# Optimization experiments

Measured on AMD Instinct MI355X. Metric: run time of the kernel, lower is better.

Reference implementation:

```python
import jax, jax.numpy as jnp
import numpy as np

L, ND, ED, AD = 2, 128, 64, 64
N, E, A, G = 50000, 300000, 600000, 16
EPS = 1e-5


def _graph_norm(h, batch, num_graphs, w, b):
    # PyG LayerNorm(mode='graph'): scalar mean/var over all nodes*features per graph.
    F = h.shape[-1]
    cnt = jax.ops.segment_sum(jnp.ones(h.shape[0], h.dtype), batch, num_segments=num_graphs)
    norm = jnp.maximum(cnt, 1.0) * F  # [G]
    mean = (jax.ops.segment_sum(h, batch, num_segments=num_graphs).sum(-1) / norm)[batch][:, None]
    hc = h - mean
    var = (jax.ops.segment_sum(hc * hc, batch, num_segments=num_graphs).sum(-1) / norm)
    out = hc * jax.lax.rsqrt(var + EPS)[batch][:, None]
    return out * w + b


def setup_inputs() -> dict:
    key = jax.random.key(0)
    ks = jax.random.split(key, 24)

    def lin(k, fi, fo):
        return jax.random.normal(k, (L, fi, fo), jnp.float32) / jnp.sqrt(float(fi))

    inp = {
        "x": jax.random.normal(ks[0], (N, ND), jnp.float32),
        "edge_attr": jax.random.normal(ks[1], (E, ED), jnp.float32),
        "angle_attr": jax.random.normal(ks[2], (A, AD), jnp.float32),
        # node_edge_mlp: [2*ND+ED -> ED], plain linear (plain_last=True)
        "W_ne": lin(ks[3], 2 * ND + ED, ED), "b_ne": jnp.zeros((L, ED), jnp.float32),
        "g_e": jnp.ones((L, ED), jnp.float32), "be_e": jnp.zeros((L, ED), jnp.float32),
        # edge_angle_mlp: [2*ED+AD -> AD]
        "W_ea": lin(ks[4], 2 * ED + AD, AD), "b_ea": jnp.zeros((L, AD), jnp.float32),
        "g_a": jnp.ones((L, AD), jnp.float32), "be_a": jnp.zeros((L, AD), jnp.float32),
        # edge_graph_mp message net: [2*ED+AD -> ED]
        "W_emp": lin(ks[5], 2 * ED + AD, ED), "b_emp": jnp.zeros((L, ED), jnp.float32),
        "g_emp": jnp.ones((L, ED), jnp.float32), "be_emp": jnp.zeros((L, ED), jnp.float32),
        # node_graph_mp message net: [2*ND+ED -> ND]
        "W_nmp": lin(ks[6], 2 * ND + ED, ND), "b_nmp": jnp.zeros((L, ND), jnp.float32),
        "g_nmp": jnp.ones((L, ND), jnp.float32), "be_nmp": jnp.zeros((L, ND), jnp.float32),
        "node_batch": jnp.sort(jax.random.randint(ks[7], (N,), 0, G)),
        "edge_index": jax.random.randint(ks[8], (2, E), 0, N),
        "edge_batch": jnp.sort(jax.random.randint(ks[9], (E,), 0, G)),
        "threebody_index": jax.random.randint(ks[10], (2, A), 0, E),
        "angle_batch": jnp.sort(jax.random.randint(ks[11], (A,), 0, G)),
        "num_graphs": G,
    }
    return inp


def reference(x, edge_attr, angle_attr,
              W_ne, b_ne, g_e, be_e,
              W_ea, b_ea, g_a, be_a,
              W_emp, b_emp, g_emp, be_emp,
              W_nmp, b_nmp, g_nmp, be_nmp,
              node_batch, edge_index, edge_batch,
              threebody_index, angle_batch, num_graphs):
    src_e, dst_e = edge_index[0], edge_index[1]
    src_t, dst_t = threebody_index[0], threebody_index[1]
    n_nodes, n_edges = x.shape[0], edge_attr.shape[0]
    for i in range(W_ne.shape[0]):
        # node-pair -> edge update + residual + graph norm
        ecat = jnp.concatenate([x[src_e], x[dst_e], edge_attr], axis=-1)
        edge_attr = edge_attr + ecat @ W_ne[i] + b_ne[i]
        edge_attr = _graph_norm(edge_attr, edge_batch, num_graphs, g_e[i], be_e[i])
        # edge-pair -> angle update + residual + graph norm
        acat = jnp.concatenate([edge_attr[src_t], edge_attr[dst_t], angle_attr], axis=-1)
        angle_attr = angle_attr + acat @ W_ea[i] + b_ea[i]
        angle_attr = _graph_norm(angle_attr, angle_batch, num_graphs, g_a[i], be_a[i])
        # edge_graph_mp: angle-mediated message passing over edges
        mcat = jnp.concatenate([edge_attr[src_t], edge_attr[dst_t], angle_attr], axis=-1)
        msg = jax.nn.relu(mcat @ W_emp[i] + b_emp[i])
        agg = jax.ops.segment_sum(msg, dst_t, num_segments=n_edges)
        edge_attr = _graph_norm(edge_attr + agg, edge_batch, num_graphs, g_emp[i], be_emp[i])
        # node_graph_mp: edge-mediated message passing over nodes
        ncat = jnp.concatenate([x[src_e], x[dst_e], edge_attr], axis=-1)
        nmsg = jax.nn.relu(ncat @ W_nmp[i] + b_nmp[i])
        nagg = jax.ops.segment_sum(nmsg, dst_e, num_segments=n_nodes)
        x = _graph_norm(x + nagg, node_batch, num_graphs, g_nmp[i], be_nmp[i])
    return x
```

## Files before the change

kernel.cpp:

```cpp
#include <hip/hip_runtime.h>

typedef __attribute__((ext_vector_type(8))) short bf16x8_t;
typedef __attribute__((ext_vector_type(4))) short bf16x4_t;
typedef __attribute__((ext_vector_type(4))) float f32x4_t;

constexpr int NG = 16;
constexpr float EPS = 1e-5f;

__device__ inline unsigned short f2bf(float f) {
  unsigned u = __builtin_bit_cast(unsigned, f);
  u += 0x7FFFu + ((u >> 16) & 1u);
  return (unsigned short)(u >> 16);
}
__device__ inline float bf2f(unsigned short u) {
  unsigned x = ((unsigned)u) << 16;
  return __builtin_bit_cast(float, x);
}

__global__ __launch_bounds__(256) void k_dense_x(
    const float* __restrict__ x,
    const unsigned short* __restrict__ WtNE,
    const unsigned short* __restrict__ WtNM,
    unsigned short* __restrict__ P, int nN)
{
  int gw = (int)((blockIdx.x * 256u + threadIdx.x) >> 6);
  int ntile = nN >> 4;
  if (gw >= ntile) return;
  int lane = threadIdx.x & 63;
  int colb = lane & 15;
  int ko = (lane >> 4) << 3;
  int rowb = (lane >> 4) << 2;
  int row = (gw << 4) + colb;
  const float* xr = x + (size_t)row * 128;
  f32x4_t a1[4] = {}, a2[4] = {}, a3[8] = {}, a4[8] = {};
#pragma unroll
  for (int c = 0; c < 4; ++c) {
    float4 f0 = *(const float4*)(xr + c * 32 + ko);
    float4 f1 = *(const float4*)(xr + c * 32 + ko + 4);
    float vv[8] = {f0.x,f0.y,f0.z,f0.w,f1.x,f1.y,f1.z,f1.w};
    bf16x8_t a;
#pragma unroll
    for (int k = 0; k < 8; ++k) a[k] = (short)f2bf(vv[k]);
#pragma unroll
    for (int nb = 0; nb < 4; ++nb) {
      bf16x8_t b1 = *(const bf16x8_t*)(WtNE + (size_t)(nb * 16 + colb) * 320 + c * 32 + ko);
      a1[nb] = __builtin_amdgcn_mfma_f32_16x16x32_bf16(a, b1, a1[nb], 0, 0, 0);
      bf16x8_t b2 = *(const bf16x8_t*)(WtNE + (size_t)(nb * 16 + colb) * 320 + (c + 4) * 32 + ko);
      a2[nb] = __builtin_amdgcn_mfma_f32_16x16x32_bf16(a, b2, a2[nb], 0, 0, 0);
    }
#pragma unroll
    for (int nb = 0; nb < 8; ++nb) {
      bf16x8_t b3 = *(const bf16x8_t*)(WtNM + (size_t)(nb * 16 + colb) * 320 + c * 32 + ko);
      a3[nb] = __builtin_amdgcn_mfma_f32_16x16x32_bf16(a, b3, a3[nb], 0, 0, 0);
      bf16x8_t b4 = *(const bf16x8_t*)(WtNM + (size_t)(nb * 16 + colb) * 320 + (c + 4) * 32 + ko);
      a4[nb] = __builtin_amdgcn_mfma_f32_16x16x32_bf16(a, b4, a4[nb], 0, 0, 0);
    }
  }
#pragma unroll
  for (int r = 0; r < 4; ++r) {
    size_t ro = (size_t)((gw << 4) + rowb + r) * 384;
    bf16x4_t t1, t2;
#pragma unroll
    for (int nb = 0; nb < 4; ++nb) { t1[nb] = (short)f2bf(a1[nb][r]); t2[nb] = (short)f2bf(a2[nb][r]); }
    *(bf16x4_t*)(P + ro + colb * 4) = t1;
    *(bf16x4_t*)(P + ro + 64 + colb * 4) = t2;
    bf16x8_t t3, t4;
#pragma unroll
    for (int nb = 0; nb < 8; ++nb) { t3[nb] = (short)f2bf(a3[nb][r]); t4[nb] = (short)f2bf(a4[nb][r]); }
    *(bf16x8_t*)(P + ro + 128 + colb * 8) = t3;
    *(bf16x8_t*)(P + ro + 256 + colb * 8) = t4;
  }
}

__global__ __launch_bounds__(256) void k_edge(
    const unsigned short* __restrict__ P, const float* e_in, float* e_out,
    const int* __restrict__ ei, const int* __restrict__ ebatch,
    const unsigned short* __restrict__ Wt,
    const float* __restrict__ bias,
    const float* __restrict__ afA, const float* __restrict__ afB,
    float* __restrict__ gs1, float* __restrict__ gs2,
    unsigned short* __restrict__ pn, int nE)
{
  __shared__ float lA[1024], lB[1024];
  __shared__ float ls1[NG], ls2[NG];
  for (int i = threadIdx.x; i < 1024; i += 256) { lA[i] = afA[i]; lB[i] = afB[i]; }
  if (threadIdx.x < NG) { ls1[threadIdx.x] = 0.f; ls2[threadIdx.x] = 0.f; }
  __syncthreads();
  int gw = (int)((blockIdx.x * 256u + threadIdx.x) >> 6);
  int ntile = nE >> 4;
  bool act = gw < ntile;
  int lane = threadIdx.x & 63;
  int colb = lane & 15;
  int ko = (lane >> 4) << 3;
  int rowb = (lane >> 4) << 2;
  float sr[4] = {0.f,0.f,0.f,0.f}, ssr[4] = {0.f,0.f,0.f,0.f};
  if (act) {
    int sI[4], dI[4];
#pragma unroll
    for (int r = 0; r < 4; ++r) {
      int e_r = (gw << 4) + rowb + r;
      sI[r] = ei[e_r]; dI[r] = ei[nE + e_r];
    }
    bf16x4_t g1[4], g2[4]; bf16x8_t g3[4], g4[4];
#pragma unroll
    for (int r = 0; r < 4; ++r) {
      g1[r] = *(const bf16x4_t*)(P + (size_t)sI[r] * 384 + colb * 4);
      g2[r] = *(const bf16x4_t*)(P + (size_t)dI[r] * 384 + 64 + colb * 4);
      g3[r] = *(const bf16x8_t*)(P + (size_t)sI[r] * 384 + 128 + colb * 8);
      g4[r] = *(const bf16x8_t*)(P + (size_t)dI[r] * 384 + 256 + colb * 8);
    }
    int row = (gw << 4) + colb;
    int ge = ebatch[row];
    const float* er = e_in + (size_t)row * 64;
    f32x4_t acc[4] = {};
#pragma unroll
    for (int c2 = 0; c2 < 2; ++c2) {
      int fb = c2 * 32 + ko;
      float4 f0 = *(const float4*)(er + fb);
      float4 f1 = *(const float4*)(er + fb + 4);
      float vv[8] = {f0.x,f0.y,f0.z,f0.w,f1.x,f1.y,f1.z,f1.w};
      bf16x8_t a;
#pragma unroll
      for (int k = 0; k < 8; ++k) a[k] = (short)f2bf(vv[k] * lA[ge*64 + fb + k] + lB[ge*64 + fb + k]);
#pragma unroll
      for (int nb = 0; nb < 4; ++nb) {
        bf16x8_t b = *(const bf16x8_t*)(Wt + (size_t)(nb * 16 + colb) * 320 + (8 + c2) * 32 + ko);
        acc[nb] = __builtin_amdgcn_mfma_f32_16x16x32_bf16(a, b, acc[nb], 0, 0, 0);
      }
    }
#pragma unroll
    for (int r = 0; r < 4; ++r) {
      int e_ = (gw << 4) + rowb + r;
      int gr = ebatch[e_];
#pragma unroll
      for (int nb = 0; nb < 4; ++nb) {
        int col = nb * 16 + colb;
        size_t off = (size_t)e_ * 64 + col;
        float vv = e_in[off] * lA[gr*64 + col] + lB[gr*64 + col] + bias[col]
                 + acc[nb][r] + bf2f((unsigned short)g1[r][nb]) + bf2f((unsigned short)g2[r][nb]);
        e_out[off] = vv;
        sr[r] += vv; ssr[r] += vv * vv;
      }
      bf16x8_t pv;
#pragma unroll
      for (int k = 0; k < 8; ++k)
        pv[k] = (short)f2bf(bf2f((unsigned short)g3[r][k]) + bf2f((unsigned short)g4[r][k]));
      *(bf16x8_t*)(pn + (size_t)e_ * 128 + colb * 8) = pv;
    }
  }
#pragma unroll
  for (int m = 1; m <= 8; m <<= 1)
#pragma unroll
    for (int r = 0; r < 4; ++r) { sr[r] += __shfl_xor(sr[r], m); ssr[r] += __shfl_xor(ssr[r], m); }
  if (act && colb == 0) {
#pragma unroll
    for (int r = 0; r < 4; ++r) {
      int g = ebatch[(gw << 4) + rowb + r];
      atomicAdd(&ls1[g], sr[r]); atomicAdd(&ls2[g], ssr[r]);
    }
  }
  __syncthreads();
  if (threadIdx.x < NG) {
    atomicAdd(&gs1[threadIdx.x], ls1[threadIdx.x]);
    atomicAdd(&gs2[threadIdx.x], ls2[threadIdx.x]);
  }
}

__global__ __launch_bounds__(256) void k_fin_nmp(
    const float* __restrict__ e, const int* __restrict__ ebatch,
    const unsigned short* __restrict__ Wt,
    const float* __restrict__ bias,
    const float* __restrict__ afEA, const float* __restrict__ afEB,
    const unsigned short* __restrict__ pn,
    unsigned short* __restrict__ msg, int nE)
{
  __shared__ float lEA[1024], lEB[1024];
  for (int i = threadIdx.x; i < 1024; i += 256) { lEA[i] = afEA[i]; lEB[i] = afEB[i]; }
  __syncthreads();
  int gw = (int)((blockIdx.x * 256u + threadIdx.x) >> 6);
  int ntile = nE >> 4;
  if (gw >= ntile) return;
  int lane = threadIdx.x & 63;
  int colb = lane & 15;
  int ko = (lane >> 4) << 3;
  int rowb = (lane >> 4) << 2;
  int row = (gw << 4) + colb;
  int ge = ebatch[row];
  const float* er = e + (size_t)row * 64;
  f32x4_t acc[8] = {};
#pragma unroll
  for (int c2 = 0; c2 < 2; ++c2) {
    int fb = c2 * 32 + ko;
    float4 f0 = *(const float4*)(er + fb);
    float4 f1 = *(const float4*)(er + fb + 4);
    float vv[8] = {f0.x,f0.y,f0.z,f0.w,f1.x,f1.y,f1.z,f1.w};
    bf16x8_t a;
#pragma unroll
    for (int k = 0; k < 8; ++k) a[k] = (short)f2bf(vv[k] * lEA[ge*64 + fb + k] + lEB[ge*64 + fb + k]);
#pragma unroll
    for (int nb = 0; nb < 8; ++nb) {
      bf16x8_t b = *(const bf16x8_t*)(Wt + (size_t)(nb * 16 + colb) * 320 + (8 + c2) * 32 + ko);
      acc[nb] = __builtin_amdgcn_mfma_f32_16x16x32_bf16(a, b, acc[nb], 0, 0, 0);
    }
  }
#pragma unroll
  for (int r = 0; r < 4; ++r) {
    int e_ = (gw << 4) + rowb + r;
    bf16x8_t p8 = *(const bf16x8_t*)(pn + (size_t)e_ * 128 + colb * 8);
#pragma unroll
    for (int nb = 0; nb < 8; ++nb) {
      int col = nb * 16 + colb;
      float v = fmaxf(acc[nb][r] + bf2f((unsigned short)p8[nb]) + bias[col], 0.f);
      msg[(size_t)e_ * 128 + col] = f2bf(v);
    }
  }
}

__global__ __launch_bounds__(256) void k_mm_angle(
    const unsigned short* __restrict__ eB1, const float* a_in, float* a_out,
    const int* __restrict__ ti, const int* __restrict__ abatch,
    const unsigned short* __restrict__ Wt, const float* __restrict__ bias,
    const float* __restrict__ afAA, const float* __restrict__ afAB,
    float* __restrict__ gs1, float* __restrict__ gs2, int nA)
{
  __shared__ float lAA[1024], lAB[1024];
  __shared__ float ls1[NG], ls2[NG];
  for (int i = threadIdx.x; i < 1024; i += 256) { lAA[i] = afAA[i]; lAB[i] = afAB[i]; }
  if (threadIdx.x < NG) { ls1[threadIdx.x] = 0.f; ls2[threadIdx.x] = 0.f; }
  __syncthreads();
  int gw = (int)((blockIdx.x * 256u + threadIdx.x) >> 6);
  int ntile = nA >> 4;
  bool act = gw < ntile;
  int lane = threadIdx.x & 63;
  int colb = lane & 15;
  int ko = (lane >> 4) << 3;
  int rowb = (lane >> 4) << 2;
  float sr[4] = {0.f,0.f,0.f,0.f}, ssr[4] = {0.f,0.f,0.f,0.f};
  if (act) {
    int row = (gw << 4) + colb;
    int s = ti[row], d = ti[nA + row];
    int ga = abatch[row];
    const unsigned short* es = eB1 + (size_t)s * 64;
    const unsigned short* ed = eB1 + (size_t)d * 64;
    const float* ar = a_in + (size_t)row * 64;
    f32x4_t acc[4] = {};
#pragma unroll
    for (int c = 0; c < 6; ++c) {
      bf16x8_t a;
      if (c < 4) {
        const unsigned short* bp = (c < 2) ? es + c * 32 : ed + (c - 2) * 32;
        a = *(const bf16x8_t*)(bp + ko);
      } else {
        int fb = (c - 4) * 32 + ko;
        float4 f0 = *(const float4*)(ar + fb);
        float4 f1 = *(const float4*)(ar + fb + 4);
        float vv[8] = {f0.x,f0.y,f0.z,f0.w,f1.x,f1.y,f1.z,f1.w};
#pragma unroll
        for (int k = 0; k < 8; ++k) a[k] = (short)f2bf(vv[k] * lAA[ga*64 + fb + k] + lAB[ga*64 + fb + k]);
      }
#pragma unroll
      for (int nb = 0; nb < 4; ++nb) {
        bf16x8_t b = *(const bf16x8_t*)(Wt + (size_t)(nb * 16 + colb) * 192 + c * 32 + ko);
        acc[nb] = __builtin_amdgcn_mfma_f32_16x16x32_bf16(a, b, acc[nb], 0, 0, 0);
      }
    }
#pragma unroll
    for (int r = 0; r < 4; ++r) {
      int a_ = (gw << 4) + rowb + r;
      int gr = abatch[a_];
#pragma unroll
      for (int nb = 0; nb < 4; ++nb) {
        int col = nb * 16 + colb;
        size_t off = (size_t)a_ * 64 + col;
        float vv = a_in[off] * lAA[gr*64 + col] + lAB[gr*64 + col] + bias[col] + acc[nb][r];
        a_out[off] = vv;
        sr[r] += vv; ssr[r] += vv * vv;
      }
    }
  }
#pragma unroll
  for (int m = 1; m <= 8; m <<= 1)
#pragma unroll
    for (int r = 0; r < 4; ++r) { sr[r] += __shfl_xor(sr[r], m); ssr[r] += __shfl_xor(ssr[r], m); }
  if (act && colb == 0) {
#pragma unroll
    for (int r = 0; r < 4; ++r) {
      int g = abatch[(gw << 4) + rowb + r];
      atomicAdd(&ls1[g], sr[r]); atomicAdd(&ls2[g], ssr[r]);
    }
  }
  __syncthreads();
  if (threadIdx.x < NG) {
    atomicAdd(&gs1[threadIdx.x], ls1[threadIdx.x]);
    atomicAdd(&gs2[threadIdx.x], ls2[threadIdx.x]);
  }
}

__global__ __launch_bounds__(256) void k_mm_emp(
    const unsigned short* __restrict__ eB1, const float* __restrict__ a_,
    const int* __restrict__ ti, const int* __restrict__ abatch,
    const unsigned short* __restrict__ Wt, const float* __restrict__ bias,
    const float* __restrict__ afAA, const float* __restrict__ afAB,
    unsigned short* __restrict__ msg, int nA)
{
  __shared__ float lAA[1024], lAB[1024];
  for (int i = threadIdx.x; i < 1024; i += 256) { lAA[i] = afAA[i]; lAB[i] = afAB[i]; }
  __syncthreads();
  int gw = (int)((blockIdx.x * 256u + threadIdx.x) >> 6);
  int ntile = nA >> 4;
  if (gw >= ntile) return;
  int lane = threadIdx.x & 63;
  int colb = lane & 15;
  int ko = (lane >> 4) << 3;
  int rowb = (lane >> 4) << 2;
  int row = (gw << 4) + colb;
  int s = ti[row], d = ti[nA + row];
  int ga = abatch[row];
  const unsigned short* es = eB1 + (size_t)s * 64;
  const unsigned short* ed = eB1 + (size_t)d * 64;
  const float* ar = a_ + (size_t)row * 64;
  f32x4_t acc[4] = {};
#pragma unroll
  for (int c = 0; c < 6; ++c) {
    bf16x8_t a;
    if (c < 4) {
      const unsigned short* bp = (c < 2) ? es + c * 32 : ed + (c - 2) * 32;
      a = *(const bf16x8_t*)(bp + ko);
    } else {
      int fb = (c - 4) * 32 + ko;
      float4 f0 = *(const float4*)(ar + fb);
      float4 f1 = *(const float4*)(ar + fb + 4);
      float vv[8] = {f0.x,f0.y,f0.z,f0.w,f1.x,f1.y,f1.z,f1.w};
#pragma unroll
      for (int k = 0; k < 8; ++k) a[k] = (short)f2bf(vv[k] * lAA[ga*64 + fb + k] + lAB[ga*64 + fb + k]);
    }
#pragma unroll
    for (int nb = 0; nb < 4; ++nb) {
      bf16x8_t b = *(const bf16x8_t*)(Wt + (size_t)(nb * 16 + colb) * 192 + c * 32 + ko);
      acc[nb] = __builtin_amdgcn_mfma_f32_16x16x32_bf16(a, b, acc[nb], 0, 0, 0);
    }
  }
#pragma unroll
  for (int r = 0; r < 4; ++r) {
    int a_idx = (gw << 4) + rowb + r;
#pragma unroll
    for (int nb = 0; nb < 4; ++nb) {
      int col = nb * 16 + colb;
      float v = fmaxf(acc[nb][r] + bias[col], 0.f);
      msg[(size_t)a_idx * 64 + col] = f2bf(v);
    }
  }
}

__global__ __launch_bounds__(256) void k_red_e(
    const unsigned short* __restrict__ msg, const float* e_in, float* e_out,
    const int* __restrict__ ptr, const int* __restrict__ perm,
    const int* __restrict__ ebatch,
    const float* __restrict__ afA, const float* __restrict__ afB,
    float* __restrict__ gs1, float* __restrict__ gs2, int nE)
{
  __shared__ float lA[1024], lB[1024], ls1[NG], ls2[NG];
  for (int i = threadIdx.x; i < 1024; i += 256) { lA[i] = afA[i]; lB[i] = afB[i]; }
  if (threadIdx.x < NG) { ls1[threadIdx.x] = 0.f; ls2[threadIdx.x] = 0.f; }
  __syncthreads();
  int lane = threadIdx.x & 63;
  int wv = (int)((blockIdx.x * 256u + threadIdx.x) >> 6);
  int nw = (int)((gridDim.x * 256u) >> 6);
  for (int eidx = wv; eidx < nE; eidx += nw) {
    int p0 = ptr[eidx], p1 = ptr[eidx + 1];
    float sum = 0.f;
    for (int j = p0; j < p1; ++j) {
      int aidx = perm[j];
      sum += bf2f(msg[(size_t)aidx * 64 + lane]);
    }
    int g = ebatch[eidx];
    size_t off = (size_t)eidx * 64 + lane;
    float v = e_in[off] * lA[g*64 + lane] + lB[g*64 + lane] + sum;
    e_out[off] = v;
    float s = v, ss = v * v;
#pragma unroll
    for (int m = 1; m < 64; m <<= 1) { s += __shfl_xor(s, m); ss += __shfl_xor(ss, m); }
    if (lane == 0) { atomicAdd(&ls1[g], s); atomicAdd(&ls2[g], ss); }
  }
  __syncthreads();
  if (threadIdx.x < NG) {
    atomicAdd(&gs1[threadIdx.x], ls1[threadIdx.x]);
    atomicAdd(&gs2[threadIdx.x], ls2[threadIdx.x]);
  }
}

__global__ __launch_bounds__(256) void k_red_n(
    const unsigned short* __restrict__ msg, const float* x_in, float* out,
    const int* __restrict__ ptr, const int* __restrict__ perm,
    const int* __restrict__ nbatch,
    float* __restrict__ gs1, float* __restrict__ gs2, int nN)
{
  __shared__ float ls1[NG], ls2[NG];
  if (threadIdx.x < NG) { ls1[threadIdx.x] = 0.f; ls2[threadIdx.x] = 0.f; }
  __syncthreads();
  int lane = threadIdx.x & 63;
  int wv = (int)((blockIdx.x * 256u + threadIdx.x) >> 6);
  int nw = (int)((gridDim.x * 256u) >> 6);
  for (int n = wv; n < nN; n += nw) {
    int p0 = ptr[n], p1 = ptr[n + 1];
    float s0 = 0.f, s1v = 0.f;
    for (int j = p0; j < p1; ++j) {
      int e = perm[j];
      unsigned u = *(const unsigned*)(msg + (size_t)e * 128 + lane * 2);
      s0 += bf2f((unsigned short)(u & 0xffffu));
      s1v += bf2f((unsigned short)(u >> 16));
    }
    size_t off = (size_t)n * 128 + lane * 2;
    float h0 = x_in[off] + s0, h1 = x_in[off + 1] + s1v;
    out[off] = h0; out[off + 1] = h1;
    float s = h0 + h1, ss = h0 * h0 + h1 * h1;
#pragma unroll
    for (int m = 1; m < 64; m <<= 1) { s += __shfl_xor(s, m); ss += __shfl_xor(ss, m); }
    if (lane == 0) { int g = nbatch[n]; atomicAdd(&ls1[g], s); atomicAdd(&ls2[g], ss); }
  }
  __syncthreads();
  if (threadIdx.x < NG) {
    atomicAdd(&gs1[threadIdx.x], ls1[threadIdx.x]);
    atomicAdd(&gs2[threadIdx.x], ls2[threadIdx.x]);
  }
}

__global__ __launch_bounds__(256) void k_mkaff(
    const float* __restrict__ s1, const float* __restrict__ s2,
    const float* __restrict__ cnt, int F,
    const float* __restrict__ w, const float* __restrict__ b,
    float* __restrict__ A, float* __restrict__ B)
{
  int idx = blockIdx.x * 256 + threadIdx.x;
  if (idx >= NG * F) return;
  int g = idx / F, f = idx - g * F;
  float norm = fmaxf(cnt[g], 1.f) * (float)F;
  float m = s1[g] / norm;
  float var = s2[g] / norm - m * m;
  float inv = rsqrtf(var + EPS);
  float a = inv * w[f];
  A[idx] = a;
  B[idx] = b[f] - m * a;
}

__global__ __launch_bounds__(256) void k_idaff(float* __restrict__ A, float* __restrict__ B, int n)
{
  int idx = blockIdx.x * 256 + threadIdx.x;
  if (idx < n) { A[idx] = 1.f; B[idx] = 0.f; }
}

__global__ __launch_bounds__(256) void k_norm_ebf(
    const float* __restrict__ e, const int* __restrict__ ebatch,
    const float* __restrict__ afA, const float* __restrict__ afB,
    unsigned short* __restrict__ eB, int nE)
{
  int total = nE * 8;
  int stride = gridDim.x * 256;
  for (int idx = blockIdx.x * 256 + threadIdx.x; idx < total; idx += stride) {
    int row = idx >> 3, q = (idx & 7) * 8;
    int g = ebatch[row];
    const float* er = e + (size_t)row * 64 + q;
    float4 f0 = *(const float4*)er;
    float4 f1 = *(const float4*)(er + 4);
    float vv[8] = {f0.x,f0.y,f0.z,f0.w,f1.x,f1.y,f1.z,f1.w};
    bf16x8_t o;
#pragma unroll
    for (int k = 0; k < 8; ++k) o[k] = (short)f2bf(vv[k] * afA[g*64 + q + k] + afB[g*64 + q + k]);
    *(bf16x8_t*)(eB + (size_t)row * 64 + q) = o;
  }
}

__global__ __launch_bounds__(256) void k_apply(
    float* h, const int* __restrict__ batch,
    const float* __restrict__ A, const float* __restrict__ B, int nN)
{
  int total = nN * 16;
  int stride = gridDim.x * 256;
  for (int idx = blockIdx.x * 256 + threadIdx.x; idx < total; idx += stride) {
    int row = idx >> 4, q = (idx & 15) * 8;
    int g = batch[row];
    float* hp = h + (size_t)row * 128 + q;
    float4 f0 = *(const float4*)hp;
    float4 f1 = *(const float4*)(hp + 4);
    float vv[8] = {f0.x,f0.y,f0.z,f0.w,f1.x,f1.y,f1.z,f1.w};
#pragma unroll
    for (int k = 0; k < 8; ++k) vv[k] = vv[k] * A[(g << 7) + q + k] + B[(g << 7) + q + k];
    float4 g0 = {vv[0],vv[1],vv[2],vv[3]}, g1 = {vv[4],vv[5],vv[6],vv[7]};
    *(float4*)hp = g0;
    *(float4*)(hp + 4) = g1;
  }
}

__global__ __launch_bounds__(256) void k_count(
    const int* __restrict__ batch, int n, float* __restrict__ cnt)
{
  __shared__ float lc[NG];
  if (threadIdx.x < NG) lc[threadIdx.x] = 0.f;
  __syncthreads();
  for (int i = blockIdx.x * 256 + threadIdx.x; i < n; i += gridDim.x * 256)
    atomicAdd(&lc[batch[i]], 1.f);
  __syncthreads();
  if (threadIdx.x < NG) atomicAdd(&cnt[threadIdx.x], lc[threadIdx.x]);
}

__global__ __launch_bounds__(256) void k_hist(
    const int* __restrict__ dst, int n, int* __restrict__ cnt)
{
  for (int i = blockIdx.x * 256 + threadIdx.x; i < n; i += gridDim.x * 256)
    atomicAdd(&cnt[dst[i]], 1);
}

__global__ __launch_bounds__(256) void k_scan1(
    const int* __restrict__ in, int* __restrict__ out, int* __restrict__ bsum, int n)
{
  __shared__ int wtot[4];
  int tid = threadIdx.x, lane = tid & 63, wid = tid >> 6;
  int base = blockIdx.x * 1024 + tid * 4;
  int v[4];
#pragma unroll
  for (int k = 0; k < 4; ++k) v[k] = (base + k < n) ? in[base + k] : 0;
  int tsum = v[0] + v[1] + v[2] + v[3];
  int incl = tsum;
// ... 64 lines not shown
    const int* __restrict__ dst, int* __restrict__ cur, int* __restrict__ perm, int n)
{
  for (int i = blockIdx.x * 256 + threadIdx.x; i < n; i += gridDim.x * 256) {
    int d = dst[i];
    int p = atomicAdd(&cur[d], 1);
    perm[p] = i;
  }
}

__global__ __launch_bounds__(256) void k_wt(
    const float* __restrict__ W, unsigned short* __restrict__ Wt, int K, int NO)
{
  int idx = blockIdx.x * 256 + threadIdx.x;
  if (idx >= K * NO) return;
  int k = idx / NO, j = idx - k * NO;
  Wt[(size_t)j * K + k] = f2bf(W[idx]);
}

extern "C" void kernel_launch(void* const* d_in, const int* in_sizes, int n_in,
                              void* d_out, int out_size, void* d_ws, size_t ws_size,
                              hipStream_t stream)
{
  const float* x0    = (const float*)d_in[0];
  const float* e0    = (const float*)d_in[1];
  const float* a0    = (const float*)d_in[2];
  const float* W_ne  = (const float*)d_in[3];
  const float* b_ne  = (const float*)d_in[4];
  const float* g_e   = (const float*)d_in[5];
  const float* be_e  = (const float*)d_in[6];
  const float* W_ea  = (const float*)d_in[7];
  const float* b_ea  = (const float*)d_in[8];
  const float* g_a   = (const float*)d_in[9];
  const float* be_a  = (const float*)d_in[10];
  const float* W_emp = (const float*)d_in[11];
  const float* b_emp = (const float*)d_in[12];
  const float* g_emp = (const float*)d_in[13];
  const float* be_emp= (const float*)d_in[14];
  const float* W_nmp = (const float*)d_in[15];
  const float* b_nmp = (const float*)d_in[16];
  const float* g_nmp = (const float*)d_in[17];
  const float* be_nmp= (const float*)d_in[18];
  const int* node_batch  = (const int*)d_in[19];
  const int* edge_index  = (const int*)d_in[20];
  const int* edge_batch  = (const int*)d_in[21];
  const int* tb_index    = (const int*)d_in[22];
  const int* angle_batch = (const int*)d_in[23];

  const int N = in_sizes[0] / 128;
  const int E = in_sizes[1] / 64;
  const int A = in_sizes[2] / 64;

  char* wsp = (char*)d_ws;
  auto alloc = [&](size_t bytes) { char* p = wsp; wsp += (bytes + 255) & ~(size_t)255; return p; };
  float*          eA     = (float*)alloc((size_t)E * 64 * 4);
  float*          aA     = (float*)alloc((size_t)A * 64 * 4);
  unsigned short* msg    = (unsigned short*)alloc((size_t)A * 64 * 2);
  unsigned short* pn     = (unsigned short*)alloc((size_t)E * 128 * 2);
  unsigned short* eB1    = (unsigned short*)alloc((size_t)E * 64 * 2);
  int* ptr_n  = (int*)alloc((size_t)(N + 1) * 4);
  int* cur_n  = (int*)alloc((size_t)N * 4);
  int* perm_n = (int*)alloc((size_t)E * 4);
  int* ptr_e  = (int*)alloc((size_t)(E + 1) * 4);
  int* cur_e  = (int*)alloc((size_t)E * 4);
  int* perm_e = (int*)alloc((size_t)A * 4);
  int* bsum   = (int*)alloc(4096 * 4);
  float* stats = (float*)alloc(5 * NG * 4);
  float* s1    = stats;
  float* s2    = stats + NG;
  float* cnt_n = stats + 2 * NG;
  float* cnt_e = stats + 3 * NG;
  float* cnt_a = stats + 4 * NG;
  float* afE_idA = (float*)alloc(1024 * 4); float* afE_idB = (float*)alloc(1024 * 4);
  float* afA_idA = (float*)alloc(1024 * 4); float* afA_idB = (float*)alloc(1024 * 4);
  float* afE1A   = (float*)alloc(1024 * 4); float* afE1B   = (float*)alloc(1024 * 4);
  float* afE2A   = (float*)alloc(1024 * 4); float* afE2B   = (float*)alloc(1024 * 4);
  float* afA1A   = (float*)alloc(1024 * 4); float* afA1B   = (float*)alloc(1024 * 4);
  float* afXA    = (float*)alloc(2048 * 4); float* afXB    = (float*)alloc(2048 * 4);
  unsigned short* wt_ne  = (unsigned short*)alloc((size_t)2 * 320 * 64 * 2);
  unsigned short* wt_ea  = (unsigned short*)alloc((size_t)2 * 192 * 64 * 2);
  unsigned short* wt_emp = (unsigned short*)alloc((size_t)2 * 192 * 64 * 2);
  unsigned short* wt_nmp = (unsigned short*)alloc((size_t)2 * 320 * 128 * 2);

  unsigned short* P = msg;
  float* x_out = (float*)d_out;

  for (int i = 0; i < 2; ++i) {
    k_wt<<<(320*64 + 255)/256, 256, 0, stream>>>(W_ne  + (size_t)i*320*64,  wt_ne  + (size_t)i*320*64,  320, 64);
    k_wt<<<(192*64 + 255)/256, 256, 0, stream>>>(W_ea  + (size_t)i*192*64,  wt_ea  + (size_t)i*192*64,  192, 64);
    k_wt<<<(192*64 + 255)/256, 256, 0, stream>>>(W_emp + (size_t)i*192*64,  wt_emp + (size_t)i*192*64,  192, 64);
    k_wt<<<(320*128 + 255)/256, 256, 0, stream>>>(W_nmp + (size_t)i*320*128, wt_nmp + (size_t)i*320*128, 320, 128);
  }
  hipMemsetAsync(stats, 0, 5 * NG * 4, stream);
  k_count<<<512, 256, 0, stream>>>(node_batch, N, cnt_n);
  k_count<<<512, 256, 0, stream>>>(edge_batch, E, cnt_e);
  k_count<<<512, 256, 0, stream>>>(angle_batch, A, cnt_a);
  k_idaff<<<4, 256, 0, stream>>>(afE_idA, afE_idB, 1024);
  k_idaff<<<4, 256, 0, stream>>>(afA_idA, afA_idB, 1024);

  hipMemsetAsync(cur_n, 0, (size_t)N * 4, stream);
  hipMemsetAsync(cur_e, 0, (size_t)E * 4, stream);
  k_hist<<<1024, 256, 0, stream>>>(edge_index + E, E, cur_n);
  k_hist<<<1024, 256, 0, stream>>>(tb_index + A, A, cur_e);
  int nbN = (N + 1023) / 1024, nbE = (E + 1023) / 1024;
  k_scan1<<<nbN, 256, 0, stream>>>(cur_n, ptr_n, bsum, N);
  k_scan2<<<1, 256, 0, stream>>>(bsum, nbN, ptr_n + N);
  k_scan3<<<1024, 256, 0, stream>>>(ptr_n, cur_n, bsum, N);
  k_scatter<<<1024, 256, 0, stream>>>(edge_index + E, cur_n, perm_n, E);
  k_scan1<<<nbE, 256, 0, stream>>>(cur_e, ptr_e, bsum, E);
  k_scan2<<<1, 256, 0, stream>>>(bsum, nbE, ptr_e + E);
  k_scan3<<<1024, 256, 0, stream>>>(ptr_e, cur_e, bsum, E);
  k_scatter<<<1024, 256, 0, stream>>>(tb_index + A, cur_e, perm_e, A);

  const float* x_cur = x0;
  int blkE = (E / 16 + 3) / 4;
  int blkA = (A / 16 + 3) / 4;
  int blkN = (N / 16 + 3) / 4;

  for (int i = 0; i < 2; ++i) {
    const float* e_in  = (i == 0) ? e0 : eA;
    const float* a_in  = (i == 0) ? a0 : aA;
    const float* fEinA = (i == 0) ? afE_idA : afE2A;
    const float* fEinB = (i == 0) ? afE_idB : afE2B;
    const float* fAinA = (i == 0) ? afA_idA : afA1A;
    const float* fAinB = (i == 0) ? afA_idB : afA1B;

    k_dense_x<<<blkN, 256, 0, stream>>>(x_cur, wt_ne + (size_t)i*320*64,
                                        wt_nmp + (size_t)i*320*128, P, N);

    hipMemsetAsync(s1, 0, 2 * NG * 4, stream);
    k_edge<<<blkE, 256, 0, stream>>>(P, e_in, eA, edge_index, edge_batch,
                                     wt_ne + (size_t)i*320*64, b_ne + i*64,
                                     fEinA, fEinB, s1, s2, pn, E);
    k_mkaff<<<4, 256, 0, stream>>>(s1, s2, cnt_e, 64, g_e + i*64, be_e + i*64, afE1A, afE1B);
    k_norm_ebf<<<2048, 256, 0, stream>>>(eA, edge_batch, afE1A, afE1B, eB1, E);

    hipMemsetAsync(s1, 0, 2 * NG * 4, stream);
    k_mm_angle<<<blkA, 256, 0, stream>>>(eB1, a_in, aA, tb_index, angle_batch,
                                         wt_ea + (size_t)i*192*64, b_ea + i*64,
                                         fAinA, fAinB, s1, s2, A);
    k_mkaff<<<4, 256, 0, stream>>>(s1, s2, cnt_a, 64, g_a + i*64, be_a + i*64, afA1A, afA1B);

    k_mm_emp<<<blkA, 256, 0, stream>>>(eB1, aA, tb_index, angle_batch,
                                       wt_emp + (size_t)i*192*64, b_emp + i*64,
                                       afA1A, afA1B, msg, A);
    hipMemsetAsync(s1, 0, 2 * NG * 4, stream);
    k_red_e<<<2048, 256, 0, stream>>>(msg, eA, eA, ptr_e, perm_e, edge_batch,
                                      afE1A, afE1B, s1, s2, E);
    k_mkaff<<<4, 256, 0, stream>>>(s1, s2, cnt_e, 64, g_emp + i*64, be_emp + i*64, afE2A, afE2B);

    k_fin_nmp<<<blkE, 256, 0, stream>>>(eA, edge_batch, wt_nmp + (size_t)i*320*128,
                                        b_nmp + i*128, afE2A, afE2B, pn, msg, E);
    hipMemsetAsync(s1, 0, 2 * NG * 4, stream);
    k_red_n<<<2048, 256, 0, stream>>>(msg, x_cur, x_out, ptr_n, perm_n, node_batch,
                                      s1, s2, N);
    k_mkaff<<<8, 256, 0, stream>>>(s1, s2, cnt_n, 128, g_nmp + i*128, be_nmp + i*128, afXA, afXB);
    k_apply<<<2048, 256, 0, stream>>>(x_out, node_batch, afXA, afXB, N);

    x_cur = x_out;
  }
}
```

Measured before the change: 1.866 ms.

## Precompute per-edge projections for emp message and store edge/angle state in bf16

Splits the emp message matmul so the edge-side terms (W·e[src], W·e[dst]) are computed once per edge in a new prep kernel, fused with the bf16 normalization that replaces k_norm_ebf. The angle kernel then gathers these precomputed partials and writes them into msg, and a slimmer k_fin_emp only multiplies the angle features. Edge and angle state buffers change from fp32 to bf16 to halve their memory traffic. In exchange, residual state loses precision and an extra E×128 bf16 buffer is needed.

```diff
diff --git a/kernel.cpp b/kernel.cpp
--- a/kernel.cpp
+++ b/kernel.cpp
@@ -15,6 +15,25 @@
 __device__ inline float bf2f(unsigned short u) {
   unsigned x = ((unsigned)u) << 16;
   return __builtin_bit_cast(float, x);
+}
+
+template<bool F32>
+__device__ inline void ldrow8(const void* base, size_t off, float v[8]) {
+  if constexpr (F32) {
+    const float* p = (const float*)base + off;
+    float4 f0 = *(const float4*)p, f1 = *(const float4*)(p + 4);
+    v[0]=f0.x; v[1]=f0.y; v[2]=f0.z; v[3]=f0.w;
+    v[4]=f1.x; v[5]=f1.y; v[6]=f1.z; v[7]=f1.w;
+  } else {
+    bf16x8_t t = *(const bf16x8_t*)((const unsigned short*)base + off);
+#pragma unroll
+    for (int k = 0; k < 8; ++k) v[k] = bf2f((unsigned short)t[k]);
+  }
+}
+template<bool F32>
+__device__ inline float ldel(const void* base, size_t off) {
+  if constexpr (F32) return ((const float*)base)[off];
+  return bf2f(((const unsigned short*)base)[off]);
 }
 
 __global__ __launch_bounds__(256) void k_dense_x(
@@ -72,8 +91,56 @@
   }
 }
 
+__global__ __launch_bounds__(256) void k_prep_e(
+    const unsigned short* __restrict__ eA, const int* __restrict__ ebatch,
+    const float* __restrict__ afA, const float* __restrict__ afB,
+    const unsigned short* __restrict__ WtP,
+    unsigned short* __restrict__ eB1, unsigned short* __restrict__ PE, int nE)
+{
+  __shared__ float lA[1024], lB[1024];
+  for (int i = threadIdx.x; i < 1024; i += 256) { lA[i] = afA[i]; lB[i] = afB[i]; }
+  __syncthreads();
+  int gw = (int)((blockIdx.x * 256u + threadIdx.x) >> 6);
+  int ntile = nE >> 4;
+  if (gw >= ntile) return;
+  int lane = threadIdx.x & 63;
+  int colb = lane & 15;
+  int ko = (lane >> 4) << 3;
+  int rowb = (lane >> 4) << 2;
+  int row = (gw << 4) + colb;
+  int ge = ebatch[row];
+  f32x4_t a3[4] = {}, a4[4] = {};
+#pragma unroll
+  for (int c2 = 0; c2 < 2; ++c2) {
+    int fb = c2 * 32 + ko;
+    bf16x8_t t = *(const bf16x8_t*)(eA + (size_t)row * 64 + fb);
+    bf16x8_t an;
+#pragma unroll
+    for (int k = 0; k < 8; ++k)
+      an[k] = (short)f2bf(bf2f((unsigned short)t[k]) * lA[ge*64 + fb + k] + lB[ge*64 + fb + k]);
+    *(bf16x8_t*)(eB1 + (size_t)row * 64 + fb) = an;
+#pragma unroll
+    for (int nb = 0; nb < 4; ++nb) {
+      bf16x8_t b3 = *(const bf16x8_t*)(WtP + (size_t)(nb * 16 + colb) * 192 + c2 * 32 + ko);
+      a3[nb] = __builtin_amdgcn_mfma_f32_16x16x32_bf16(an, b3, a3[nb], 0, 0, 0);
+      bf16x8_t b4 = *(const bf16x8_t*)(WtP + (size_t)(nb * 16 + colb) * 192 + 64 + c2 * 32 + ko);
+      a4[nb] = __builtin_amdgcn_mfma_f32_16x16x32_bf16(an, b4, a4[nb], 0, 0, 0);
+    }
+  }
+#pragma unroll
+  for (int r = 0; r < 4; ++r) {
+    size_t ro = (size_t)((gw << 4) + rowb + r) * 128;
+    bf16x4_t t3, t4;
+#pragma unroll
+    for (int nb = 0; nb < 4; ++nb) { t3[nb] = (short)f2bf(a3[nb][r]); t4[nb] = (short)f2bf(a4[nb][r]); }
+    *(bf16x4_t*)(PE + ro + colb * 4) = t3;
+    *(bf16x4_t*)(PE + ro + 64 + colb * 4) = t4;
+  }
+}
+
+template<bool EF32>
 __global__ __launch_bounds__(256) void k_edge(
-    const unsigned short* __restrict__ P, const float* e_in, float* e_out,
+    const unsigned short* __restrict__ P, const void* e_in, unsigned short* e_out,
     const int* __restrict__ ei, const int* __restrict__ ebatch,
     const unsigned short* __restrict__ Wt,
     const float* __restrict__ bias,
@@ -111,14 +178,12 @@
     }
     int row = (gw << 4) + colb;
     int ge = ebatch[row];
-    const float* er = e_in + (size_t)row * 64;
     f32x4_t acc[4] = {};
 #pragma unroll
     for (int c2 = 0; c2 < 2; ++c2) {
       int fb = c2 * 32 + ko;
-      float4 f0 = *(const float4*)(er + fb);
-      float4 f1 = *(const float4*)(er + fb + 4);
-      float vv[8] = {f0.x,f0.y,f0.z,f0.w,f1.x,f1.y,f1.z,f1.w};
+      float vv[8];
+      ldrow8<EF32>(e_in, (size_t)row * 64 + fb, vv);
       bf16x8_t a;
 #pragma unroll
       for (int k = 0; k < 8; ++k) a[k] = (short)f2bf(vv[k] * lA[ge*64 + fb + k] + lB[ge*64 + fb + k]);
@@ -136,9 +201,10 @@
       for (int nb = 0; nb < 4; ++nb) {
         int col = nb * 16 + colb;
         size_t off = (size_t)e_ * 64 + col;
-        float vv = e_in[off] * lA[gr*64 + col] + lB[gr*64 + col] + bias[col]
+        float ev = ldel<EF32>(e_in, off);
+        float vv = ev * lA[gr*64 + col] + lB[gr*64 + col] + bias[col]
                  + acc[nb][r] + bf2f((unsigned short)g1[r][nb]) + bf2f((unsigned short)g2[r][nb]);
-        e_out[off] = vv;
+        e_out[off] = f2bf(vv);
         sr[r] += vv; ssr[r] += vv * vv;
       }
       bf16x8_t pv;
@@ -166,8 +232,157 @@
   }
 }
 
+template<bool AF32>
+__global__ __launch_bounds__(256) void k_angle(
+    const unsigned short* __restrict__ eB1, const unsigned short* __restrict__ PE,
+    const void* a_in, unsigned short* a_out,
+    const int* __restrict__ ti, const int* __restrict__ abatch,
+    const unsigned short* __restrict__ Wt, const float* __restrict__ bias,
+    const float* __restrict__ afAA, const float* __restrict__ afAB,
+    float* __restrict__ gs1, float* __restrict__ gs2,
+    unsigned short* __restrict__ pe, int nA)
+{
+  __shared__ float lAA[1024], lAB[1024];
+  __shared__ float ls1[NG], ls2[NG];
+  for (int i = threadIdx.x; i < 1024; i += 256) { lAA[i] = afAA[i]; lAB[i] = afAB[i]; }
+  if (threadIdx.x < NG) { ls1[threadIdx.x] = 0.f; ls2[threadIdx.x] = 0.f; }
+  __syncthreads();
+  int gw = (int)((blockIdx.x * 256u + threadIdx.x) >> 6);
+  int ntile = nA >> 4;
+  bool act = gw < ntile;
+  int lane = threadIdx.x & 63;
+  int colb = lane & 15;
+  int ko = (lane >> 4) << 3;
+  int rowb = (lane >> 4) << 2;
+  float sr[4] = {0.f,0.f,0.f,0.f}, ssr[4] = {0.f,0.f,0.f,0.f};
+  if (act) {
+    int sI[4], dI[4];
+#pragma unroll
+    for (int r = 0; r < 4; ++r) {
+      int a_r = (gw << 4) + rowb + r;
+      sI[r] = ti[a_r]; dI[r] = ti[nA + a_r];
+    }
+    bf16x4_t g3[4], g4[4];
+#pragma unroll
+    for (int r = 0; r < 4; ++r) {
+      g3[r] = *(const bf16x4_t*)(PE + (size_t)sI[r] * 128 + colb * 4);
+      g4[r] = *(const bf16x4_t*)(PE + (size_t)dI[r] * 128 + 64 + colb * 4);
+    }
+    int row = (gw << 4) + colb;
+    int s = ti[row], d = ti[nA + row];
+    int ga = abatch[row];
+    const unsigned short* es = eB1 + (size_t)s * 64;
+    const unsigned short* ed = eB1 + (size_t)d * 64;
+    f32x4_t acc[4] = {};
+#pragma unroll
+    for (int c = 0; c < 6; ++c) {
+      bf16x8_t a;
+      if (c < 4) {
+        const unsigned short* bp = (c < 2) ? es + c * 32 : ed + (c - 2) * 32;
+        a = *(const bf16x8_t*)(bp + ko);
+      } else {
+        int fb = (c - 4) * 32 + ko;
+        float vv[8];
+        ldrow8<AF32>(a_in, (size_t)row * 64 + fb, vv);
+#pragma unroll
+        for (int k = 0; k < 8; ++k) a[k] = (short)f2bf(vv[k] * lAA[ga*64 + fb + k] + lAB[ga*64 + fb + k]);
+      }
+#pragma unroll
+      for (int nb = 0; nb < 4; ++nb) {
+        bf16x8_t b = *(const bf16x8_t*)(Wt + (size_t)(nb * 16 + colb) * 192 + c * 32 + ko);
+        acc[nb] = __builtin_amdgcn_mfma_f32_16x16x32_bf16(a, b, acc[nb], 0, 0, 0);
+      }
+    }
+#pragma unroll
+    for (int r = 0; r < 4; ++r) {
+      int a_ = (gw << 4) + rowb + r;
+      int gr = abatch[a_];
+#pragma unroll
+      for (int nb = 0; nb < 4; ++nb) {
+        int col = nb * 16 + colb;
+        size_t off = (size_t)a_ * 64 + col;
+        float av = ldel<AF32>(a_in, off);
+        float vv = av * lAA[gr*64 + col] + lAB[gr*64 + col] + bias[col] + acc[nb][r];
+        a_out[off] = f2bf(vv);
+        sr[r] += vv; ssr[r] += vv * vv;
+      }
+      bf16x4_t pv;
+#pragma unroll
+      for (int nb = 0; nb < 4; ++nb)
+        pv[nb] = (short)f2bf(bf2f((unsigned short)g3[r][nb]) + bf2f((unsigned short)g4[r][nb]));
+      *(bf16x4_t*)(pe + (size_t)a_ * 64 + colb * 4) = pv;
+    }
+  }
+#pragma unroll
+  for (int m = 1; m <= 8; m <<= 1)
+#pragma unroll
+    for (int r = 0; r < 4; ++r) { sr[r] += __shfl_xor(sr[r], m); ssr[r] += __shfl_xor(ssr[r], m); }
+  if (act && colb == 0) {
+#pragma unroll
+    for (int r = 0; r < 4; ++r) {
+      int g = abatch[(gw << 4) + rowb + r];
+      atomicAdd(&ls1[g], sr[r]); atomicAdd(&ls2[g], ssr[r]);
+    }
+  }
+  __syncthreads();
+  if (threadIdx.x < NG) {
+    atomicAdd(&gs1[threadIdx.x], ls1[threadIdx.x]);
+    atomicAdd(&gs2[threadIdx.x], ls2[threadIdx.x]);
+  }
+}
+
+__global__ __launch_bounds__(256) void k_fin_emp(
+    const unsigned short* __restrict__ a_, const int* __restrict__ abatch,
+    const unsigned short* __restrict__ Wt,
+    const float* __restrict__ bias,
+    const float* __restrict__ afAA, const float* __restrict__ afAB,
+    unsigned short* __restrict__ msg, int nA)
+{
+  __shared__ float lAA[1024], lAB[1024];
+  for (int i = threadIdx.x; i < 1024; i += 256) { lAA[i] = afAA[i]; lAB[i] = afAB[i]; }
+  __syncthreads();
+  int gw = (int)((blockIdx.x * 256u + threadIdx.x) >> 6);
+  int ntile = nA >> 4;
+  if (gw >= ntile) return;
+  int lane = threadIdx.x & 63;
+  int colb = lane & 15;
+  int ko = (lane >> 4) << 3;
+  int rowb = (lane >> 4) << 2;
+  int row = (gw << 4) + colb;
+  int ga = abatch[row];
+  f32x4_t acc[4] = {};
+#pragma unroll
+  for (int c2 = 0; c2 < 2; ++c2) {
+    int fb = c2 * 32 + ko;
+    bf16x8_t t = *(const bf16x8_t*)(a_ + (size_t)row * 64 + fb);
+    bf16x8_t a;
+#pragma unroll
+    for (int k = 0; k < 8; ++k)
+      a[k] = (short)f2bf(bf2f((unsigned short)t[k]) * lAA[ga*64 + fb + k] + lAB[ga*64 + fb + k]);
+#pragma unroll
+    for (int nb = 0; nb < 4; ++nb) {
+      bf16x8_t b = *(const bf16x8_t*)(Wt + (size_t)(nb * 16 + colb) * 192 + 128 + c2 * 32 + ko);
+      acc[nb] = __builtin_amdgcn_mfma_f32_16x16x32_bf16(a, b, acc[nb], 0, 0, 0);
+    }
+  }
+  bf16x4_t p4[4];
+#pragma unroll
+  for (int r = 0; r < 4; ++r)
+    p4[r] = *(const bf16x4_t*)(msg + (size_t)((gw << 4) + rowb + r) * 64 + colb * 4);
+#pragma unroll
+  for (int r = 0; r < 4; ++r) {
+    int a_idx = (gw << 4) + rowb + r;
+#pragma unroll
+    for (int nb = 0; nb < 4; ++nb) {
+      int col = nb * 16 + colb;
+      float v = fmaxf(acc[nb][r] + bf2f((unsigned short)p4[r][nb]) + bias[col], 0.f);
+      msg[(size_t)a_idx * 64 + col] = f2bf(v);
+    }
+  }
+}
+
 __global__ __launch_bounds__(256) void k_fin_nmp(
-    const float* __restrict__ e, const int* __restrict__ ebatch,
+    const unsigned short* __restrict__ e, const int* __restrict__ ebatch,
     const unsigned short* __restrict__ Wt,
     const float* __restrict__ bias,
     const float* __restrict__ afEA, const float* __restrict__ afEB,
@@ -186,17 +401,15 @@
   int rowb = (lane >> 4) << 2;
   int row = (gw << 4) + colb;
   int ge = ebatch[row];
-  const float* er = e + (size_t)row * 64;
   f32x4_t acc[8] = {};
 #pragma unroll
   for (int c2 = 0; c2 < 2; ++c2) {
     int fb = c2 * 32 + ko;
-    float4 f0 = *(const float4*)(er + fb);
-    float4 f1 = *(const float4*)(er + fb + 4);
-    float vv[8] = {f0.x,f0.y,f0.z,f0.w,f1.x,f1.y,f1.z,f1.w};
+    bf16x8_t t = *(const bf16x8_t*)(e + (size_t)row * 64 + fb);
     bf16x8_t a;
 #pragma unroll
-    for (int k = 0; k < 8; ++k) a[k] = (short)f2bf(vv[k] * lEA[ge*64 + fb + k] + lEB[ge*64 + fb + k]);
+    for (int k = 0; k < 8; ++k)
+      a[k] = (short)f2bf(bf2f((unsigned short)t[k]) * lEA[ge*64 + fb + k] + lEB[ge*64 + fb + k]);
 #pragma unroll
     for (int nb = 0; nb < 8; ++nb) {
       bf16x8_t b = *(const bf16x8_t*)(Wt + (size_t)(nb * 16 + colb) * 320 + (8 + c2) * 32 + ko);
@@ -216,144 +429,8 @@
   }
 }
 
-__global__ __launch_bounds__(256) void k_mm_angle(
-    const unsigned short* __restrict__ eB1, const float* a_in, float* a_out,
-    const int* __restrict__ ti, const int* __restrict__ abatch,
-    const unsigned short* __restrict__ Wt, const float* __restrict__ bias,
-    const float* __restrict__ afAA, const float* __restrict__ afAB,
-    float* __restrict__ gs1, float* __restrict__ gs2, int nA)
-{
-  __shared__ float lAA[1024], lAB[1024];
-  __shared__ float ls1[NG], ls2[NG];
-  for (int i = threadIdx.x; i < 1024; i += 256) { lAA[i] = afAA[i]; lAB[i] = afAB[i]; }
-  if (threadIdx.x < NG) { ls1[threadIdx.x] = 0.f; ls2[threadIdx.x] = 0.f; }
-  __syncthreads();
-  int gw = (int)((blockIdx.x * 256u + threadIdx.x) >> 6);
-  int ntile = nA >> 4;
-  bool act = gw < ntile;
-  int lane = threadIdx.x & 63;
-  int colb = lane & 15;
-  int ko = (lane >> 4) << 3;
-  int rowb = (lane >> 4) << 2;
-  float sr[4] = {0.f,0.f,0.f,0.f}, ssr[4] = {0.f,0.f,0.f,0.f};
-  if (act) {
-    int row = (gw << 4) + colb;
-    int s = ti[row], d = ti[nA + row];
-    int ga = abatch[row];
-    const unsigned short* es = eB1 + (size_t)s * 64;
-    const unsigned short* ed = eB1 + (size_t)d * 64;
-    const float* ar = a_in + (size_t)row * 64;
-    f32x4_t acc[4] = {};
-#pragma unroll
-    for (int c = 0; c < 6; ++c) {
-      bf16x8_t a;
-      if (c < 4) {
-        const unsigned short* bp = (c < 2) ? es + c * 32 : ed + (c - 2) * 32;
-        a = *(const bf16x8_t*)(bp + ko);
-      } else {
-        int fb = (c - 4) * 32 + ko;
-        float4 f0 = *(const float4*)(ar + fb);
-        float4 f1 = *(const float4*)(ar + fb + 4);
-        float vv[8] = {f0.x,f0.y,f0.z,f0.w,f1.x,f1.y,f1.z,f1.w};
-#pragma unroll
-        for (int k = 0; k < 8; ++k) a[k] = (short)f2bf(vv[k] * lAA[ga*64 + fb + k] + lAB[ga*64 + fb + k]);
-      }
-#pragma unroll
-      for (int nb = 0; nb < 4; ++nb) {
-        bf16x8_t b = *(const bf16x8_t*)(Wt + (size_t)(nb * 16 + colb) * 192 + c * 32 + ko);
-        acc[nb] = __builtin_amdgcn_mfma_f32_16x16x32_bf16(a, b, acc[nb], 0, 0, 0);
-      }
-    }
-#pragma unroll
-    for (int r = 0; r < 4; ++r) {
-      int a_ = (gw << 4) + rowb + r;
-      int gr = abatch[a_];
-#pragma unroll
-      for (int nb = 0; nb < 4; ++nb) {
-        int col = nb * 16 + colb;
-        size_t off = (size_t)a_ * 64 + col;
-        float vv = a_in[off] * lAA[gr*64 + col] + lAB[gr*64 + col] + bias[col] + acc[nb][r];
-        a_out[off] = vv;
-        sr[r] += vv; ssr[r] += vv * vv;
-      }
-    }
-  }
-#pragma unroll
-  for (int m = 1; m <= 8; m <<= 1)
-#pragma unroll
-    for (int r = 0; r < 4; ++r) { sr[r] += __shfl_xor(sr[r], m); ssr[r] += __shfl_xor(ssr[r], m); }
-  if (act && colb == 0) {
-#pragma unroll
-    for (int r = 0; r < 4; ++r) {
-      int g = abatch[(gw << 4) + rowb + r];
-      atomicAdd(&ls1[g], sr[r]); atomicAdd(&ls2[g], ssr[r]);
-    }
-  }
-  __syncthreads();
-  if (threadIdx.x < NG) {
-    atomicAdd(&gs1[threadIdx.x], ls1[threadIdx.x]);
-    atomicAdd(&gs2[threadIdx.x], ls2[threadIdx.x]);
-  }
-}
-
-__global__ __launch_bounds__(256) void k_mm_emp(
-    const unsigned short* __restrict__ eB1, const float* __restrict__ a_,
-    const int* __restrict__ ti, const int* __restrict__ abatch,
-    const unsigned short* __restrict__ Wt, const float* __restrict__ bias,
-    const float* __restrict__ afAA, const float* __restrict__ afAB,
-    unsigned short* __restrict__ msg, int nA)
-{
-  __shared__ float lAA[1024], lAB[1024];
-  for (int i = threadIdx.x; i < 1024; i += 256) { lAA[i] = afAA[i]; lAB[i] = afAB[i]; }
-  __syncthreads();
-  int gw = (int)((blockIdx.x * 256u + threadIdx.x) >> 6);
-  int ntile = nA >> 4;
-  if (gw >= ntile) return;
-  int lane = threadIdx.x & 63;
-  int colb = lane & 15;
-  int ko = (lane >> 4) << 3;
-  int rowb = (lane >> 4) << 2;
-  int row = (gw << 4) + colb;
-  int s = ti[row], d = ti[nA + row];
-  int ga = abatch[row];
-  const unsigned short* es = eB1 + (size_t)s * 64;
-  const unsigned short* ed = eB1 + (size_t)d * 64;
-  const float* ar = a_ + (size_t)row * 64;
-  f32x4_t acc[4] = {};
-#pragma unroll
-  for (int c = 0; c < 6; ++c) {
-    bf16x8_t a;
-    if (c < 4) {
-      const unsigned short* bp = (c < 2) ? es + c * 32 : ed + (c - 2) * 32;
-      a = *(const bf16x8_t*)(bp + ko);
-    } else {
-      int fb = (c - 4) * 32 + ko;
-      float4 f0 = *(const float4*)(ar + fb);
-      float4 f1 = *(const float4*)(ar + fb + 4);
-      float vv[8] = {f0.x,f0.y,f0.z,f0.w,f1.x,f1.y,f1.z,f1.w};
-#pragma unroll
-      for (int k = 0; k < 8; ++k) a[k] = (short)f2bf(vv[k] * lAA[ga*64 + fb + k] + lAB[ga*64 + fb + k]);
-    }
-#pragma unroll
-    for (int nb = 0; nb < 4; ++nb) {
-      bf16x8_t b = *(const bf16x8_t*)(Wt + (size_t)(nb * 16 + colb) * 192 + c * 32 + ko);
-      acc[nb] = __builtin_amdgcn_mfma_f32_16x16x32_bf16(a, b, acc[nb], 0, 0, 0);
-    }
-  }
-#pragma unroll
-  for (int r = 0; r < 4; ++r) {
-    int a_idx = (gw << 4) + rowb + r;
-#pragma unroll
-    for (int nb = 0; nb < 4; ++nb) {
-      int col = nb * 16 + colb;
-      float v = fmaxf(acc[nb][r] + bias[col], 0.f);
-      msg[(size_t)a_idx * 64 + col] = f2bf(v);
-    }
-  }
-}
-
 __global__ __launch_bounds__(256) void k_red_e(
-    const unsigned short* __restrict__ msg, const float* e_in, float* e_out,
+    const unsigned short* __restrict__ msg, const unsigned short* e_in, unsigned short* e_out,
     const int* __restrict__ ptr, const int* __restrict__ perm,
     const int* __restrict__ ebatch,
     const float* __restrict__ afA, const float* __restrict__ afB,
@@ -375,8 +452,8 @@
     }
     int g = ebatch[eidx];
     size_t off = (size_t)eidx * 64 + lane;
-    float v = e_in[off] * lA[g*64 + lane] + lB[g*64 + lane] + sum;
-    e_out[off] = v;
+    float v = bf2f(e_in[off]) * lA[g*64 + lane] + lB[g*64 + lane] + sum;
+    e_out[off] = f2bf(v);
     float s = v, ss = v * v;
 #pragma unroll
     for (int m = 1; m < 64; m <<= 1) { s += __shfl_xor(s, m); ss += __shfl_xor(ss, m); }
@@ -447,27 +524,6 @@
 {
   int idx = blockIdx.x * 256 + threadIdx.x;
   if (idx < n) { A[idx] = 1.f; B[idx] = 0.f; }
-}
-
-__global__ __launch_bounds__(256) void k_norm_ebf(
-    const float* __restrict__ e, const int* __restrict__ ebatch,
-    const float* __restrict__ afA, const float* __restrict__ afB,
-    unsigned short* __restrict__ eB, int nE)
-{
-  int total = nE * 8;
-  int stride = gridDim.x * 256;
-  for (int idx = blockIdx.x * 256 + threadIdx.x; idx < total; idx += stride) {
-    int row = idx >> 3, q = (idx & 7) * 8;
-    int g = ebatch[row];
-    const float* er = e + (size_t)row * 64 + q;
-    float4 f0 = *(const float4*)er;
-    float4 f1 = *(const float4*)(er + 4);
-    float vv[8] = {f0.x,f0.y,f0.z,f0.w,f1.x,f1.y,f1.z,f1.w};
-    bf16x8_t o;
-#pragma unroll
-    for (int k = 0; k < 8; ++k) o[k] = (short)f2bf(vv[k] * afA[g*64 + q + k] + afB[g*64 + q + k]);
-    *(bf16x8_t*)(eB + (size_t)row * 64 + q) = o;
-  }
 }
 
 __global__ __launch_bounds__(256) void k_apply(
@@ -638,11 +694,12 @@
 
   char* wsp = (char*)d_ws;
   auto alloc = [&](size_t bytes) { char* p = wsp; wsp += (bytes + 255) & ~(size_t)255; return p; };
-  float*          eA     = (float*)alloc((size_t)E * 64 * 4);
-  float*          aA     = (float*)alloc((size_t)A * 64 * 4);
-  unsigned short* msg    = (unsigned short*)alloc((size_t)A * 64 * 2);
-  unsigned short* pn     = (unsigned short*)alloc((size_t)E * 128 * 2);
-  unsigned short* eB1    = (unsigned short*)alloc((size_t)E * 64 * 2);
+  unsigned short* eAB  = (unsigned short*)alloc((size_t)E * 64 * 2);
+  unsigned short* aAB  = (unsigned short*)alloc((size_t)A * 64 * 2);
+  unsigned short* msg  = (unsigned short*)alloc((size_t)A * 64 * 2);
+  unsigned short* pn   = (unsigned short*)alloc((size_t)E * 128 * 2);
+  unsigned short* eB1  = (unsigned short*)alloc((size_t)E * 64 * 2);
+  unsigned short* PE   = (unsigned short*)alloc((size_t)E * 128 * 2);
   int* ptr_n  = (int*)alloc((size_t)(N + 1) * 4);
   int* cur_n  = (int*)alloc((size_t)N * 4);
   int* perm_n = (int*)alloc((size_t)E * 4);
@@ -703,8 +760,6 @@
   int blkN = (N / 16 + 3) / 4;
 
   for (int i = 0; i < 2; ++i) {
-    const float* e_in  = (i == 0) ? e0 : eA;
-    const float* a_in  = (i == 0) ? a0 : aA;
     const float* fEinA = (i == 0) ? afE_idA : afE2A;
     const float* fEinB = (i == 0) ? afE_idB : afE2B;
     const float* fAinA = (i == 0) ? afA_idA : afA1A;
@@ -714,27 +769,38 @@
                                         wt_nmp + (size_t)i*320*128, P, N);
 
     hipMemsetAsync(s1, 0, 2 * NG * 4, stream);
-    k_edge<<<blkE, 256, 0, stream>>>(P, e_in, eA, edge_index, edge_batch,
-                                     wt_ne + (size_t)i*320*64, b_ne + i*64,
-                                     fEinA, fEinB, s1, s2, pn, E);
+    if (i == 0)
+      k_edge<true><<<blkE, 256, 0, stream>>>(P, (const void*)e0, eAB, edge_index, edge_batch,
+                                             wt_ne + (size_t)i*320*64, b_ne + i*64,
+                                             fEinA, fEinB, s1, s2, pn, E);
+    else
+      k_edge<false><<<blkE, 256, 0, stream>>>(P, (const void*)eAB, eAB, edge_index, edge_batch,
+                                              wt_ne + (size_t)i*320*64, b_ne + i*64,
+                                              fEinA, fEinB, s1, s2, pn, E);
     k_mkaff<<<4, 256, 0, stream>>>(s1, s2, cnt_e, 64, g_e + i*64, be_e + i*64, afE1A, afE1B);
-    k_norm_ebf<<<2048, 256, 0, stream>>>(eA, edge_batch, afE1A, afE1B, eB1, E);
+
+    k_prep_e<<<blkE, 256, 0, stream>>>(eAB, edge_batch, afE1A, afE1B,
+                                       wt_emp + (size_t)i*192*64, eB1, PE, E);
 
     hipMemsetAsync(s1, 0, 2 * NG * 4, stream);
-    k_mm_angle<<<blkA, 256, 0, stream>>>(eB1, a_in, aA, tb_index, angle_batch,
-                                         wt_ea + (size_t)i*192*64, b_ea + i*64,
-                                         fAinA, fAinB, s1, s2, A);
+    if (i == 0)
+      k_angle<true><<<blkA, 256, 0, stream>>>(eB1, PE, (const void*)a0, aAB, tb_index, angle_batch,
+                                              wt_ea + (size_t)i*192*64, b_ea + i*64,
+                                              fAinA, fAinB, s1, s2, msg, A);
+    else
+      k_angle<false><<<blkA, 256, 0, stream>>>(eB1, PE, (const void*)aAB, aAB, tb_index, angle_batch,
+                                               wt_ea + (size_t)i*192*64, b_ea + i*64,
+                                               fAinA, fAinB, s1, s2, msg, A);
     k_mkaff<<<4, 256, 0, stream>>>(s1, s2, cnt_a, 64, g_a + i*64, be_a + i*64, afA1A, afA1B);
 
-    k_mm_emp<<<blkA, 256, 0, stream>>>(eB1, aA, tb_index, angle_batch,
-                                       wt_emp + (size_t)i*192*64, b_emp + i*64,
-                                       afA1A, afA1B, msg, A);
+    k_fin_emp<<<blkA, 256, 0, stream>>>(aAB, angle_batch, wt_emp + (size_t)i*192*64,
+                                        b_emp + i*64, afA1A, afA1B, msg, A);
     hipMemsetAsync(s1, 0, 2 * NG * 4, stream);
-    k_red_e<<<2048, 256, 0, stream>>>(msg, eA, eA, ptr_e, perm_e, edge_batch,
+    k_red_e<<<2048, 256, 0, stream>>>(msg, eAB, eAB, ptr_e, perm_e, edge_batch,
                                       afE1A, afE1B, s1, s2, E);
     k_mkaff<<<4, 256, 0, stream>>>(s1, s2, cnt_e, 64, g_emp + i*64, be_emp + i*64, afE2A, afE2B);
 
-    k_fin_nmp<<<blkE, 256, 0, stream>>>(eA, edge_batch, wt_nmp + (size_t)i*320*128,
+    k_fin_nmp<<<blkE, 256, 0, stream>>>(eAB, edge_batch, wt_nmp + (size_t)i*320*128,
                                         b_nmp + i*128, afE2A, afE2B, pn, msg, E);
     hipMemsetAsync(s1, 0, 2 * NG * 4, stream);
     k_red_n<<<2048, 256, 0, stream>>>(msg, x_cur, x_out, ptr_n, perm_n, node_batch,
```

Result: faster. 1.712 ms (-8.3%).
